# Optimization experiments

Measured on AMD Instinct MI355X. Metric: run time of the kernel, lower is better.

The kernel has to match this reference:

```python
import jax, jax.numpy as jnp
import numpy as np

D_MODEL = 2048
HEAD_DIM = 128

def setup_inputs() -> dict:
    key = jax.random.key(0)
    ks = jax.random.split(key, 7)
    s = 1.0 / np.sqrt(D_MODEL)
    x = jax.random.normal(ks[0], (4, 4096, D_MODEL), dtype=jnp.float32)
    Wq = jax.random.uniform(ks[1], (D_MODEL, HEAD_DIM), jnp.float32, -s, s)
    bq = jax.random.uniform(ks[2], (HEAD_DIM,), jnp.float32, -s, s)
    Wk = jax.random.uniform(ks[3], (D_MODEL, HEAD_DIM), jnp.float32, -s, s)
    bk = jax.random.uniform(ks[4], (HEAD_DIM,), jnp.float32, -s, s)
    Wv = jax.random.uniform(ks[5], (D_MODEL, HEAD_DIM), jnp.float32, -s, s)
    bv = jax.random.uniform(ks[6], (HEAD_DIM,), jnp.float32, -s, s)
    return {"x": x, "Wq": Wq, "bq": bq, "Wk": Wk, "bk": bk, "Wv": Wv, "bv": bv}

def reference(x, Wq, bq, Wk, bk, Wv, bv):
    # x: [B, T, d_model]
    B, T, _ = x.shape
    q = jnp.einsum('btd,dh->bth', x, Wq) + bq  # [B,T,H]
    k = jnp.einsum('btd,dh->bth', x, Wk) + bk
    v = jnp.einsum('btd,dh->bth', x, Wv) + bv
    scores = jnp.einsum('bth,bsh->bts', q, k) / jnp.sqrt(jnp.float32(HEAD_DIM))  # [B,T,T]
    causal = jnp.tril(jnp.ones((T, T), dtype=bool))
    scores = jnp.where(causal[None], scores, -jnp.inf)
    probs = jax.nn.softmax(scores, axis=-1)
    return jnp.einsum('bts,bsh->bth', probs, v)  # [B,T,H]
```

## Files before the change

kernel.cpp:

```cpp
#include <hip/hip_runtime.h>
#include <math.h>

#define D_MODEL 2048
#define HD      128
#define NB      4
#define TT      4096
#define M_TOT   (NB * TT)
#define NCH     160
#define CHT     16

typedef __attribute__((ext_vector_type(8))) short bf16x8;
typedef __attribute__((ext_vector_type(4))) float f32x4;

__device__ __forceinline__ ushort f2bf(float f) {
    union { float f; unsigned int u; } v; v.f = f;
    unsigned int u = v.u;
    unsigned int r = (u + 0x7FFFu + ((u >> 16) & 1u)) >> 16;
    return (ushort)r;
}

__device__ __forceinline__ void gload_lds16(const void* g, void* l) {
    __builtin_amdgcn_global_load_lds(
        (const __attribute__((address_space(1))) unsigned int*)g,
        (__attribute__((address_space(3))) unsigned int*)l, 16, 0, 0);
}

__global__ __launch_bounds__(256) void wt_kernel(
        const float* __restrict__ Wq, const float* __restrict__ Wk,
        const float* __restrict__ Wv, ushort* __restrict__ WT) {
    const int p  = blockIdx.y;
    const int k0 = blockIdx.x * 128;
    const float* W = (p == 0) ? Wq : ((p == 1) ? Wk : Wv);

    __shared__ ushort Ts[128 * 136];

    const int tid = threadIdx.x;
    for (int i = 0; i < 64; i++) {
        int c  = i * 256 + tid;
        int kk = c >> 7, n = c & 127;
        Ts[n * 136 + kk] = f2bf(W[(size_t)(k0 + kk) * 128 + n]);
    }
    __syncthreads();
    for (int i = 0; i < 8; i++) {
        int c = i * 256 + tid;
        int n = c >> 4, j = c & 15;
        *(uint4*)(WT + (size_t)p * (128 * 2048) + (size_t)n * 2048 + k0 + j * 8) =
            *(const uint4*)&Ts[n * 136 + j * 8];
    }
}

__global__ __launch_bounds__(256, 3) void proj_fused(
        const float* __restrict__ x, const ushort* __restrict__ WT,
        const float* __restrict__ bq, const float* __restrict__ bk, const float* __restrict__ bv,
        ushort* __restrict__ Qb, ushort* __restrict__ Kb, ushort* __restrict__ Vt) {
    const int bx0  = blockIdx.x;
    const int l    = (bx0 & 7) * 96 + (bx0 >> 3);
    const int row0 = (l / 3) * 64;
    const int p    = l % 3;
    const ushort* Wp   = WT + (size_t)p * (128 * 2048);
    const float*  bias = (p == 0) ? bq : ((p == 1) ? bk : bv);

    __shared__ ushort As[64 * 136];
    __shared__ ushort Bs[128 * 128];

    const int tid  = threadIdx.x;
    const int lane = tid & 63;
    const int wv   = tid >> 6;
    const int rw   = wv >> 1;
    const int cw   = wv & 1;
    const int quad = lane >> 4;
    const int ln16 = lane & 15;

    size_t  boff[8];
    ushort* bdst[8];
    for (int i = 0; i < 8; i++) {
        int c = i * 256 + tid;
        int n = c >> 4, j = c & 15;
        int kc = j ^ (n & 15);
        boff[i] = (size_t)n * 2048 + kc * 8;
        bdst[i] = &Bs[(i * 256 + wv * 64) * 8];
    }
    int arow[8], apos[8];
    for (int i = 0; i < 8; i++) {
        int c = i * 256 + tid;
        arow[i] = c >> 5;
        apos[i] = c & 31;
    }

    f32x4 acc[2][4];
    for (int m2 = 0; m2 < 2; m2++)
        for (int nt = 0; nt < 4; nt++)
            acc[m2][nt] = (f32x4){0.f, 0.f, 0.f, 0.f};

    float4 areg[8];
    for (int i = 0; i < 8; i++)
        areg[i] = *(const float4*)(x + (size_t)(row0 + arow[i]) * D_MODEL + apos[i] * 4);

    for (int k0 = 0; k0 < D_MODEL; k0 += 128) {
        __syncthreads();
        for (int i = 0; i < 8; i++)
            gload_lds16(Wp + boff[i] + k0, bdst[i]);
        for (int i = 0; i < 8; i++) {
            ushort4 o;
            o.x = f2bf(areg[i].x); o.y = f2bf(areg[i].y);
            o.z = f2bf(areg[i].z); o.w = f2bf(areg[i].w);
            *(ushort4*)&As[arow[i] * 136 + apos[i] * 4] = o;
        }
        __syncthreads();
        if (k0 + 128 < D_MODEL)
            for (int i = 0; i < 8; i++)
                areg[i] = *(const float4*)(x + (size_t)(row0 + arow[i]) * D_MODEL
                                             + k0 + 128 + apos[i] * 4);

        for (int mi = 0; mi < 4; mi++) {
            bf16x8 a[2], b[4];
            for (int m2 = 0; m2 < 2; m2++)
                a[m2] = *(const bf16x8*)&As[(rw * 32 + m2 * 16 + ln16) * 136 + mi * 32 + quad * 8];
            for (int nt = 0; nt < 4; nt++) {
                int n = cw * 64 + nt * 16 + ln16;
                int slot = (mi * 4 + quad) ^ (n & 15);
                b[nt] = *(const bf16x8*)&Bs[n * 128 + slot * 8];
            }
            for (int m2 = 0; m2 < 2; m2++)
                for (int nt = 0; nt < 4; nt++)
                    acc[m2][nt] = __builtin_amdgcn_mfma_f32_16x16x32_bf16(a[m2], b[nt], acc[m2][nt], 0, 0, 0);
        }
    }

    for (int nt = 0; nt < 4; nt++) {
        int h  = cw * 64 + nt * 16 + ln16;
        float bc = bias[h];
        for (int m2 = 0; m2 < 2; m2++) {
            int rbase = row0 + rw * 32 + m2 * 16 + quad * 4;
            if (p < 2) {
                ushort* O = (p == 0) ? Qb : Kb;
                for (int r = 0; r < 4; r++)
                    O[(size_t)(rbase + r) * HD + h] = f2bf(acc[m2][nt][r] + bc);
            } else {
                int b = rbase >> 12;
                int t = rbase & 4095;
                ushort4 o;
                o.x = f2bf(acc[m2][nt][0] + bc);
                o.y = f2bf(acc[m2][nt][1] + bc);
                o.z = f2bf(acc[m2][nt][2] + bc);
                o.w = f2bf(acc[m2][nt][3] + bc);
                *(ushort4*)(Vt + ((size_t)b * HD + h) * TT + t) = o;
            }
        }
    }
}

#define SCALE2 0.12751744573223862f

__global__ __launch_bounds__(256, 2) void attn_part(
        const ushort* __restrict__ Qb, const ushort* __restrict__ Kb,
        const ushort* __restrict__ Vt, float* __restrict__ Opart,
        float* __restrict__ Mpart, float* __restrict__ Lpart) {
    const int blk = blockIdx.x;
    const int bb  = blk & 3;
    const int cid = blk >> 2;

    int rem = cid, qt = 63;
    for (;;) {
        int cnt = (qt >> 4) + 1;
        if (rem < cnt) break;
        rem -= cnt; --qt;
    }
    const int ch    = rem;
    const int st_lo = ch * CHT;
    const int st_hi = min(qt + 1, st_lo + CHT);
    const int q0    = qt * 64;

    __shared__ ushort Ks[2][64 * 128];
    __shared__ ushort Vs[2][128 * 64];
    __shared__ ushort Ps[64 * 64];

    const int tid  = threadIdx.x;
    const int lane = tid & 63;
    const int wv   = tid >> 6;
    const int quad = lane >> 4;
    const int ln16 = lane & 15;
    const int sw8  = ln16 & 7;

    int koff[4], voff[4], ldso[4];
    for (int i = 0; i < 4; i++) {
        int c = i * 256 + tid;
        { int r = c >> 4, j = c & 15, kc = j ^ (r & 15);
          koff[i] = r * HD + kc * 8; }
        { int h = c >> 3, j = c & 7, kc = j ^ (h & 7);
          voff[i] = h * TT + kc * 8; }
        ldso[i] = (i * 256 + wv * 64) * 8;
    }
    const ushort* kbase = Kb + (size_t)bb * TT * HD;
    const ushort* vbase = Vt + (size_t)bb * HD * TT;

    {
        const int s0 = st_lo * 64;
        for (int i = 0; i < 4; i++) gload_lds16(kbase + (size_t)s0 * HD + koff[i], &Ks[0][ldso[i]]);
        for (int i = 0; i < 4; i++) gload_lds16(vbase + s0 + voff[i], &Vs[0][ldso[i]]);
    }
    bf16x8 qf[4];
    {
        const ushort* qrow = Qb + (size_t)(bb * TT + q0 + 16 * wv + ln16) * HD;
        for (int kc = 0; kc < 4; kc++)
            qf[kc] = *(const bf16x8*)(qrow + kc * 32 + quad * 8);
    }

    f32x4 o_acc[8];
    for (int nt = 0; nt < 8; nt++) o_acc[nt] = (f32x4){0.f, 0.f, 0.f, 0.f};
    float lsum[4];
    for (int r = 0; r < 4; r++) lsum[r] = 0.f;

    __syncthreads();

    for (int st = st_lo; st < st_hi; st++) {
        const int s0  = st * 64;
        const int buf = (st - st_lo) & 1;

        if (st + 1 < st_hi) {
            const int s1 = s0 + 64;
            for (int i = 0; i < 4; i++) gload_lds16(kbase + (size_t)s1 * HD + koff[i], &Ks[buf ^ 1][ldso[i]]);
            for (int i = 0; i < 4; i++) gload_lds16(vbase + s1 + voff[i], &Vs[buf ^ 1][ldso[i]]);
        }

        f32x4 sacc[4];
        for (int nt = 0; nt < 4; nt++) sacc[nt] = (f32x4){0.f, 0.f, 0.f, 0.f};
        for (int kc = 0; kc < 4; kc++) {
            int lc = kc * 4 + quad;
            for (int nt = 0; nt < 4; nt++) {
                int r = nt * 16 + ln16;
                bf16x8 b = *(const bf16x8*)&Ks[buf][r * 128 + ((lc ^ ln16) * 8)];
                sacc[nt] = __builtin_amdgcn_mfma_f32_16x16x32_bf16(qf[kc], b, sacc[nt], 0, 0, 0);
            }
        }

        const bool diag = (st == qt);
        for (int r = 0; r < 4; r++) {
            for (int nt = 0; nt < 4; nt++) {
                float s = sacc[nt][r] * SCALE2;
                if (diag) {
                    int sg = s0 + nt * 16 + ln16;
                    int qg = q0 + 16 * wv + quad * 4 + r;
                    if (sg > qg) s = -INFINITY;
                }
                float pv = exp2f(s);
                sacc[nt][r] = pv;
                lsum[r] += pv;
            }
        }

        for (int nt = 0; nt < 4; nt++)
            for (int r = 0; r < 4; r++) {
                int row = 16 * wv + quad * 4 + r;
                int cj  = nt * 2 + (ln16 >> 3);
                Ps[row * 64 + ((cj ^ (row & 7)) * 8) + sw8] = f2bf(sacc[nt][r]);
            }

        for (int kc2 = 0; kc2 < 2; kc2++) {
            int lc = kc2 * 4 + quad;
            int prow = 16 * wv + ln16;
            bf16x8 a = *(const bf16x8*)&Ps[prow * 64 + ((lc ^ sw8) * 8)];
            for (int nt = 0; nt < 8; nt++) {
                int h = nt * 16 + ln16;
                bf16x8 b = *(const bf16x8*)&Vs[buf][h * 64 + ((lc ^ sw8) * 8)];
                o_acc[nt] = __builtin_amdgcn_mfma_f32_16x16x32_bf16(a, b, o_acc[nt], 0, 0, 0);
            }
        }

        __syncthreads();
    }

    for (int off = 8; off >= 1; off >>= 1)
        for (int r = 0; r < 4; r++)
            lsum[r] += __shfl_xor(lsum[r], off);

    const size_t slot = (size_t)bb * NCH + cid;
    for (int nt = 0; nt < 8; nt++)
        for (int r = 0; r < 4; r++)
            Opart[(slot * 64 + 16 * wv + quad * 4 + r) * HD + nt * 16 + ln16] = o_acc[nt][r];
    if (ln16 == 0)
        for (int r = 0; r < 4; r++) {
            Mpart[slot * 64 + 16 * wv + quad * 4 + r] = 0.f;
            Lpart[slot * 64 + 16 * wv + quad * 4 + r] = lsum[r];
        }
}

__global__ __launch_bounds__(256) void merge_kernel(
        const float* __restrict__ Opart, const float* __restrict__ Mpart,
        const float* __restrict__ Lpart, float* __restrict__ out) {
    const int qt = blockIdx.x;
    const int bb = blockIdx.y;
    const int nch = (qt >> 4) + 1;
    int base = 0;
    for (int q = 63; q > qt; --q) base += (q >> 4) + 1;

    const int tid = threadIdx.x;
    const int q0  = qt * 64;
    for (int e = tid; e < 64 * 32; e += 256) {
        int row = e >> 5;
        int c4  = e & 31;
        float M = -INFINITY;
        float mv[4];
        for (int ch = 0; ch < nch; ch++) {
            mv[ch] = Mpart[((size_t)bb * NCH + base + ch) * 64 + row];
            M = fmaxf(M, mv[ch]);
        }
        float L = 0.f;
        float w[4];
        for (int ch = 0; ch < nch; ch++) {
            w[ch] = __expf(mv[ch] - M);
            L += w[ch] * Lpart[((size_t)bb * NCH + base + ch) * 64 + row];
        }
        float4 acc = {0.f, 0.f, 0.f, 0.f};
        for (int ch = 0; ch < nch; ch++) {
            const float4 o = *(const float4*)(Opart +
                (((size_t)bb * NCH + base + ch) * 64 + row) * HD + c4 * 4);
            acc.x += w[ch] * o.x; acc.y += w[ch] * o.y;
            acc.z += w[ch] * o.z; acc.w += w[ch] * o.w;
        }
        float invL = 1.f / L;
        float4 res = {acc.x * invL, acc.y * invL, acc.z * invL, acc.w * invL};
        *(float4*)(out + ((size_t)bb * TT + q0 + row) * HD + c4 * 4) = res;
    }
}

extern "C" void kernel_launch(void* const* d_in, const int* in_sizes, int n_in,
                              void* d_out, int out_size, void* d_ws, size_t ws_size,
                              hipStream_t stream) {
    const float* x  = (const float*)d_in[0];
    const float* Wq = (const float*)d_in[1];
    const float* bq = (const float*)d_in[2];
    const float* Wk = (const float*)d_in[3];
    const float* bk = (const float*)d_in[4];
    const float* Wv = (const float*)d_in[5];
    const float* bv = (const float*)d_in[6];
    float* out = (float*)d_out;

    ushort* WT = (ushort*)d_ws;
    ushort* Qb = WT + (size_t)3 * HD * D_MODEL;
    ushort* Kb = Qb + (size_t)M_TOT * HD;
    ushort* Vt = Kb + (size_t)M_TOT * HD;
    float* Opart = (float*)(Vt + (size_t)M_TOT * HD);
    float* Mpart = Opart + (size_t)NB * NCH * 64 * HD;
    float* Lpart = Mpart + (size_t)NB * NCH * 64;

    hipLaunchKernelGGL(wt_kernel, dim3(16, 3), dim3(256), 0, stream, Wq, Wk, Wv, WT);
    hipLaunchKernelGGL(proj_fused, dim3(768), dim3(256), 0, stream,
                       x, WT, bq, bk, bv, Qb, Kb, Vt);
    hipLaunchKernelGGL(attn_part, dim3(NB * NCH), dim3(256), 0, stream,
                       Qb, Kb, Vt, Opart, Mpart, Lpart);
    hipLaunchKernelGGL(merge_kernel, dim3(64, NB), dim3(256), 0, stream,
                       Opart, Mpart, Lpart, out);
}
```

Before: 306.6 us.

## Widen attention blocks to 128 query rows with 8 waves sharing K/V tiles

The attention kernel now processes 128 query rows per block using 512 threads (8 waves), so each K/V tile loaded into LDS is reused by twice as many query rows and each thread issues half as many async loads. The chunk schedule, diagonal masking, partial-output layout and merge indexing are updated to the 128-row tiling. The block count halves to 320 and the diagonal mask now applies to the last two KV tiles. The risks are fewer blocks to fill the GPU, lower occupancy from the larger LDS footprint and the aggressive launch bound, and more masked work on diagonal tiles.

```diff
diff --git a/kernel.cpp b/kernel.cpp
--- a/kernel.cpp
+++ b/kernel.cpp
@@ -6,7 +6,7 @@
 #define NB      4
 #define TT      4096
 #define M_TOT   (NB * TT)
-#define NCH     160
+#define NCHB    80
 #define CHT     16
 
 typedef __attribute__((ext_vector_type(8))) short bf16x8;
@@ -152,7 +152,7 @@
 
 #define SCALE2 0.12751744573223862f
 
-__global__ __launch_bounds__(256, 2) void attn_part(
+__global__ __launch_bounds__(512, 4) void attn_part(
         const ushort* __restrict__ Qb, const ushort* __restrict__ Kb,
         const ushort* __restrict__ Vt, float* __restrict__ Opart,
         float* __restrict__ Mpart, float* __restrict__ Lpart) {
@@ -160,20 +160,20 @@
     const int bb  = blk & 3;
     const int cid = blk >> 2;
 
-    int rem = cid, qt = 63;
+    int rem = cid, qt2 = 31;
     for (;;) {
-        int cnt = (qt >> 4) + 1;
+        int cnt = (2 * qt2 + 17) >> 4;
         if (rem < cnt) break;
-        rem -= cnt; --qt;
+        rem -= cnt; --qt2;
     }
     const int ch    = rem;
     const int st_lo = ch * CHT;
-    const int st_hi = min(qt + 1, st_lo + CHT);
-    const int q0    = qt * 64;
+    const int st_hi = min(2 * qt2 + 2, st_lo + CHT);
+    const int q0    = qt2 * 128;
 
     __shared__ ushort Ks[2][64 * 128];
     __shared__ ushort Vs[2][128 * 64];
-    __shared__ ushort Ps[64 * 64];
+    __shared__ ushort Ps[128 * 64];
 
     const int tid  = threadIdx.x;
     const int lane = tid & 63;
@@ -182,22 +182,22 @@
     const int ln16 = lane & 15;
     const int sw8  = ln16 & 7;
 
-    int koff[4], voff[4], ldso[4];
-    for (int i = 0; i < 4; i++) {
-        int c = i * 256 + tid;
+    int koff[2], voff[2], ldso[2];
+    for (int i = 0; i < 2; i++) {
+        int c = i * 512 + tid;
         { int r = c >> 4, j = c & 15, kc = j ^ (r & 15);
           koff[i] = r * HD + kc * 8; }
         { int h = c >> 3, j = c & 7, kc = j ^ (h & 7);
           voff[i] = h * TT + kc * 8; }
-        ldso[i] = (i * 256 + wv * 64) * 8;
+        ldso[i] = (i * 512 + wv * 64) * 8;
     }
     const ushort* kbase = Kb + (size_t)bb * TT * HD;
     const ushort* vbase = Vt + (size_t)bb * HD * TT;
 
     {
         const int s0 = st_lo * 64;
-        for (int i = 0; i < 4; i++) gload_lds16(kbase + (size_t)s0 * HD + koff[i], &Ks[0][ldso[i]]);
-        for (int i = 0; i < 4; i++) gload_lds16(vbase + s0 + voff[i], &Vs[0][ldso[i]]);
+        for (int i = 0; i < 2; i++) gload_lds16(kbase + (size_t)s0 * HD + koff[i], &Ks[0][ldso[i]]);
+        for (int i = 0; i < 2; i++) gload_lds16(vbase + s0 + voff[i], &Vs[0][ldso[i]]);
     }
     bf16x8 qf[4];
     {
@@ -219,8 +219,8 @@
 
         if (st + 1 < st_hi) {
             const int s1 = s0 + 64;
-            for (int i = 0; i < 4; i++) gload_lds16(kbase + (size_t)s1 * HD + koff[i], &Ks[buf ^ 1][ldso[i]]);
-            for (int i = 0; i < 4; i++) gload_lds16(vbase + s1 + voff[i], &Vs[buf ^ 1][ldso[i]]);
+            for (int i = 0; i < 2; i++) gload_lds16(kbase + (size_t)s1 * HD + koff[i], &Ks[buf ^ 1][ldso[i]]);
+            for (int i = 0; i < 2; i++) gload_lds16(vbase + s1 + voff[i], &Vs[buf ^ 1][ldso[i]]);
         }
 
         f32x4 sacc[4];
@@ -234,7 +234,7 @@
             }
         }
 
-        const bool diag = (st == qt);
+        const bool diag = (st >= 2 * qt2);
         for (int r = 0; r < 4; r++) {
             for (int nt = 0; nt < 4; nt++) {
                 float s = sacc[nt][r] * SCALE2;
@@ -274,47 +274,50 @@
         for (int r = 0; r < 4; r++)
             lsum[r] += __shfl_xor(lsum[r], off);
 
-    const size_t slot = (size_t)bb * NCH + cid;
+    const size_t slot = (size_t)bb * NCHB + cid;
     for (int nt = 0; nt < 8; nt++)
         for (int r = 0; r < 4; r++)
-            Opart[(slot * 64 + 16 * wv + quad * 4 + r) * HD + nt * 16 + ln16] = o_acc[nt][r];
+            Opart[(slot * 128 + 16 * wv + quad * 4 + r) * HD + nt * 16 + ln16] = o_acc[nt][r];
     if (ln16 == 0)
         for (int r = 0; r < 4; r++) {
-            Mpart[slot * 64 + 16 * wv + quad * 4 + r] = 0.f;
-            Lpart[slot * 64 + 16 * wv + quad * 4 + r] = lsum[r];
+            Mpart[slot * 128 + 16 * wv + quad * 4 + r] = 0.f;
+            Lpart[slot * 128 + 16 * wv + quad * 4 + r] = lsum[r];
         }
 }
 
 __global__ __launch_bounds__(256) void merge_kernel(
         const float* __restrict__ Opart, const float* __restrict__ Mpart,
         const float* __restrict__ Lpart, float* __restrict__ out) {
-    const int qt = blockIdx.x;
-    const int bb = blockIdx.y;
-    const int nch = (qt >> 4) + 1;
+    const int qt  = blockIdx.x;
+    const int bb  = blockIdx.y;
+    const int qt2 = qt >> 1;
+    const int rh  = (qt & 1) * 64;
+    const int nch = (2 * qt2 + 17) >> 4;
     int base = 0;
-    for (int q = 63; q > qt; --q) base += (q >> 4) + 1;
+    for (int j = 31; j > qt2; --j) base += (2 * j + 17) >> 4;
 
     const int tid = threadIdx.x;
     const int q0  = qt * 64;
     for (int e = tid; e < 64 * 32; e += 256) {
         int row = e >> 5;
         int c4  = e & 31;
+        int srow = rh + row;
         float M = -INFINITY;
         float mv[4];
         for (int ch = 0; ch < nch; ch++) {
-            mv[ch] = Mpart[((size_t)bb * NCH + base + ch) * 64 + row];
+            mv[ch] = Mpart[((size_t)bb * NCHB + base + ch) * 128 + srow];
             M = fmaxf(M, mv[ch]);
         }
         float L = 0.f;
         float w[4];
         for (int ch = 0; ch < nch; ch++) {
             w[ch] = __expf(mv[ch] - M);
-            L += w[ch] * Lpart[((size_t)bb * NCH + base + ch) * 64 + row];
+            L += w[ch] * Lpart[((size_t)bb * NCHB + base + ch) * 128 + srow];
         }
         float4 acc = {0.f, 0.f, 0.f, 0.f};
         for (int ch = 0; ch < nch; ch++) {
             const float4 o = *(const float4*)(Opart +
-                (((size_t)bb * NCH + base + ch) * 64 + row) * HD + c4 * 4);
+                (((size_t)bb * NCHB + base + ch) * 128 + srow) * HD + c4 * 4);
             acc.x += w[ch] * o.x; acc.y += w[ch] * o.y;
             acc.z += w[ch] * o.z; acc.w += w[ch] * o.w;
         }
@@ -341,13 +344,13 @@
     ushort* Kb = Qb + (size_t)M_TOT * HD;
     ushort* Vt = Kb + (size_t)M_TOT * HD;
     float* Opart = (float*)(Vt + (size_t)M_TOT * HD);
-    float* Mpart = Opart + (size_t)NB * NCH * 64 * HD;
-    float* Lpart = Mpart + (size_t)NB * NCH * 64;
+    float* Mpart = Opart + (size_t)NB * NCHB * 128 * HD;
+    float* Lpart = Mpart + (size_t)NB * NCHB * 128;
 
     hipLaunchKernelGGL(wt_kernel, dim3(16, 3), dim3(256), 0, stream, Wq, Wk, Wv, WT);
     hipLaunchKernelGGL(proj_fused, dim3(768), dim3(256), 0, stream,
                        x, WT, bq, bk, bv, Qb, Kb, Vt);
-    hipLaunchKernelGGL(attn_part, dim3(NB * NCH), dim3(256), 0, stream,
+    hipLaunchKernelGGL(attn_part, dim3(NB * NCHB), dim3(512), 0, stream,
                        Qb, Kb, Vt, Opart, Mpart, Lpart);
     hipLaunchKernelGGL(merge_kernel, dim3(64, NB), dim3(256), 0, stream,
                        Opart, Mpart, Lpart, out);
```

New measurement: 296.9 us. -3.2%, faster.
